# Optimization experiments

Measured on AMD Instinct MI355X. Metric: run time of the kernel, lower is better.

Reference implementation:

```python
import jax, jax.numpy as jnp
import numpy as np

B, H, KLEN, D = 32, 8, 8192, 64  # batch, heads, kv_len, head_dim


def setup_inputs() -> dict:
    key = jax.random.key(0)
    k1, k2, k3, k4 = jax.random.split(key, 4)
    std = 1.0 / D ** 0.5
    Q = jax.random.normal(k1, (B, H, 1, D), dtype=jnp.float32)
    K = jax.random.normal(k2, (B, H, KLEN, D), dtype=jnp.float32)
    W_c = jax.random.normal(k3, (H, 2 * D, D), dtype=jnp.float32) * std
    W_o = jax.random.normal(k4, (H, D, 1), dtype=jnp.float32) * std
    bias = jnp.zeros((H, 1, D), dtype=jnp.float32)
    return {"Q": Q, "K": K, "W_c": W_c, "W_o": W_o, "bias": bias}


def reference(Q, K, W_c, W_o, bias):
    # concat score (NAIS, He et al. 2018)
    Qe = jnp.broadcast_to(Q, K.shape)                       # [b,h,k,d]
    QK_cat = jnp.concatenate([Qe, K], axis=-1)              # [b,h,k,2d]
    hidden = jax.nn.relu(
        jnp.einsum('bhke,hed->bhkd', QK_cat, W_c) + bias    # bias [h,1,d] broadcasts
    )                                                        # [b,h,k,d]
    scores = jnp.einsum('bhkd,hde->bhk', hidden, W_o)       # sums over d and e(=1)
    return scores
```

## Files before the change

kernel.cpp:

```cpp
#include <hip/hip_runtime.h>
#include <stdint.h>

#define B_    32
#define H_    8
#define KLEN_ 8192
#define D_    64
#define SPLIT 8
#define ROWS_PER_BLOCK (KLEN_ / SPLIT)
#define WAVES 4
#define ITERS (ROWS_PER_BLOCK / (WAVES * 16))

typedef __attribute__((ext_vector_type(8))) short short8;
typedef __attribute__((ext_vector_type(4))) float float4v;

static __device__ inline unsigned short f2bf(float f) {
    uint32_t u = __builtin_bit_cast(uint32_t, f);
    u += 0x7fffu + ((u >> 16) & 1u);
    return (unsigned short)(u >> 16);
}

__global__ __launch_bounds__(256) void nais_score_kernel(
    const float* __restrict__ Q,
    const float* __restrict__ K,
    const float* __restrict__ Wc,
    const float* __restrict__ Wo,
    const float* __restrict__ bias,
    float* __restrict__ out)
{
    const int blk   = blockIdx.x;
    const int bh    = blk / SPLIT;
    const int split = blk % SPLIT;
    const int h     = bh % H_;
    const int tid   = threadIdx.x;
    const int lane  = tid & 63;
    const int wave  = tid >> 6;
    const int c     = lane & 15;
    const int q     = lane >> 4;

    __shared__ float s_qb[D_];
    __shared__ float s_wo[D_];

    if (tid < D_) {
        const float* qv = Q + (size_t)bh * D_;
        const float* wq = Wc + (size_t)h * (2 * D_ * D_);
        float acc = bias[h * D_ + tid];
        #pragma unroll 8
        for (int e = 0; e < D_; ++e)
            acc += qv[e] * wq[e * D_ + tid];
        s_qb[tid] = acc;
        s_wo[tid] = Wo[h * D_ + tid];
    }
    __syncthreads();

    const float* wk = Wc + (size_t)h * (2 * D_ * D_) + D_ * D_;
    short8 bfrag[4][2];
    #pragma unroll
    for (int t = 0; t < 4; ++t) {
        const int d = t * 16 + c;
        #pragma unroll
        for (int half = 0; half < 2; ++half) {
            short8 f;
            #pragma unroll
            for (int j = 0; j < 8; ++j) {
                const int e = half * 32 + q * 8 + j;
                f[j] = (short)f2bf(wk[e * D_ + d]);
            }
            bfrag[t][half] = f;
        }
    }

    float qbl[4], wol[4];
    #pragma unroll
    for (int t = 0; t < 4; ++t) {
        qbl[t] = s_qb[t * 16 + c];
        wol[t] = s_wo[t * 16 + c];
    }

    const float* Kb = K + (size_t)bh * KLEN_ * D_ + (size_t)split * ROWS_PER_BLOCK * D_;
    float*       ob = out + (size_t)bh * KLEN_ + (size_t)split * ROWS_PER_BLOCK;

    for (int it = 0; it < ITERS; ++it) {
        const int krow = (it * WAVES + wave) * 16;
        const float* arow = Kb + (size_t)(krow + c) * D_ + q * 8;
        float4v a0lo = *(const float4v*)(arow);
        float4v a0hi = *(const float4v*)(arow + 4);
        float4v a1lo = *(const float4v*)(arow + 32);
        float4v a1hi = *(const float4v*)(arow + 36);
        short8 af0, af1;
        #pragma unroll
        for (int j = 0; j < 4; ++j) {
            af0[j]     = (short)f2bf(a0lo[j]);
            af0[j + 4] = (short)f2bf(a0hi[j]);
            af1[j]     = (short)f2bf(a1lo[j]);
            af1[j + 4] = (short)f2bf(a1hi[j]);
        }

        float4v pr = {0.f, 0.f, 0.f, 0.f};
        #pragma unroll
        for (int t = 0; t < 4; ++t) {
            float4v acc = {0.f, 0.f, 0.f, 0.f};
            acc = __builtin_amdgcn_mfma_f32_16x16x32_bf16(af0, bfrag[t][0], acc, 0, 0, 0);
            acc = __builtin_amdgcn_mfma_f32_16x16x32_bf16(af1, bfrag[t][1], acc, 0, 0, 0);
            #pragma unroll
            for (int r = 0; r < 4; ++r) {
                float hv = acc[r] + qbl[t];
                hv = fmaxf(hv, 0.f);
                pr[r] += hv * wol[t];
            }
        }

        #pragma unroll
        for (int r = 0; r < 4; ++r) {
            float v = pr[r];
            v += __shfl_xor(v, 1);
            v += __shfl_xor(v, 2);
            v += __shfl_xor(v, 4);
            v += __shfl_xor(v, 8);
            if (c == r) ob[krow + q * 4 + r] = v;
        }
    }
}

extern "C" void kernel_launch(void* const* d_in, const int* in_sizes, int n_in,
                              void* d_out, int out_size, void* d_ws, size_t ws_size,
                              hipStream_t stream) {
    const float* Q    = (const float*)d_in[0];
    const float* K    = (const float*)d_in[1];
    const float* Wc   = (const float*)d_in[2];
    const float* Wo   = (const float*)d_in[3];
    const float* bias = (const float*)d_in[4];
    float* out = (float*)d_out;

    dim3 grid(B_ * H_ * SPLIT);
    dim3 block(256);
    nais_score_kernel<<<grid, block, 0, stream>>>(Q, K, Wc, Wo, bias, out);
}
```

Measured before the change: 694.8 us.

## Coalesce K loads via LDS transpose, prefetch next tile, double split count

Each wave now reads its 16-row K tile with fully coalesced contiguous float4 loads, converts to bf16 with a cheaper round-half-up pack via v_perm, and writes the tile into a padded per-wave LDS buffer. It then reads MFMA A-fragments back from LDS. The next tile is register-prefetched while the current one is processed, and SPLIT doubles to launch more blocks. This targets memory latency and uncoalesced global access in a bandwidth-bound kernel, at the cost of LDS traffic. The bf16 rounding changes slightly from round-to-nearest-even to round-half-up.

```diff
diff --git a/kernel.cpp b/kernel.cpp
--- a/kernel.cpp
+++ b/kernel.cpp
@@ -5,18 +5,22 @@
 #define H_    8
 #define KLEN_ 8192
 #define D_    64
-#define SPLIT 8
+#define SPLIT 16
 #define ROWS_PER_BLOCK (KLEN_ / SPLIT)
 #define WAVES 4
-#define ITERS (ROWS_PER_BLOCK / (WAVES * 16))
+#define TILES (ROWS_PER_BLOCK / (WAVES * 16))
+
+#define LDS_ROW 144
 
 typedef __attribute__((ext_vector_type(8))) short short8;
 typedef __attribute__((ext_vector_type(4))) float float4v;
+typedef __attribute__((ext_vector_type(4))) unsigned int uint4v;
+typedef __attribute__((ext_vector_type(2))) unsigned int uint2v;
 
-static __device__ inline unsigned short f2bf(float f) {
-    uint32_t u = __builtin_bit_cast(uint32_t, f);
-    u += 0x7fffu + ((u >> 16) & 1u);
-    return (unsigned short)(u >> 16);
+static __device__ inline unsigned int pack_bf16(float x0, float x1) {
+    unsigned int a = __builtin_bit_cast(unsigned int, x0) + 0x8000u;
+    unsigned int b = __builtin_bit_cast(unsigned int, x1) + 0x8000u;
+    return __builtin_amdgcn_perm(b, a, 0x07060302u);
 }
 
 __global__ __launch_bounds__(256) void nais_score_kernel(
@@ -39,6 +43,7 @@
 
     __shared__ float s_qb[D_];
     __shared__ float s_wo[D_];
+    __shared__ unsigned char s_tile[WAVES][16 * LDS_ROW] __attribute__((aligned(16)));
 
     if (tid < D_) {
         const float* qv = Q + (size_t)bh * D_;
@@ -59,13 +64,13 @@
         const int d = t * 16 + c;
         #pragma unroll
         for (int half = 0; half < 2; ++half) {
-            short8 f;
+            uint4v f;
             #pragma unroll
-            for (int j = 0; j < 8; ++j) {
-                const int e = half * 32 + q * 8 + j;
-                f[j] = (short)f2bf(wk[e * D_ + d]);
+            for (int j2 = 0; j2 < 4; ++j2) {
+                const int e = half * 32 + q * 8 + 2 * j2;
+                f[j2] = pack_bf16(wk[(size_t)e * D_ + d], wk[(size_t)(e + 1) * D_ + d]);
             }
-            bfrag[t][half] = f;
+            bfrag[t][half] = __builtin_bit_cast(short8, f);
         }
     }
 
@@ -78,37 +83,49 @@
 
     const float* Kb = K + (size_t)bh * KLEN_ * D_ + (size_t)split * ROWS_PER_BLOCK * D_;
     float*       ob = out + (size_t)bh * KLEN_ + (size_t)split * ROWS_PER_BLOCK;
+    unsigned char* myTile = s_tile[wave];
 
-    for (int it = 0; it < ITERS; ++it) {
-        const int krow = (it * WAVES + wave) * 16;
-        const float* arow = Kb + (size_t)(krow + c) * D_ + q * 8;
-        float4v a0lo = *(const float4v*)(arow);
-        float4v a0hi = *(const float4v*)(arow + 4);
-        float4v a1lo = *(const float4v*)(arow + 32);
-        float4v a1hi = *(const float4v*)(arow + 36);
-        short8 af0, af1;
+    #define TILE_PTR(t) (Kb + (size_t)(((t) * WAVES + wave) * 16) * D_)
+
+    float4v st[2][4];
+    #pragma unroll
+    for (int j = 0; j < 4; ++j)
+        st[0][j] = *(const float4v*)(TILE_PTR(0) + j * 256 + lane * 4);
+
+    for (int t = 0; t < TILES; ++t) {
+        const int cb = t & 1, nb = cb ^ 1;
+        if (t + 1 < TILES) {
+            #pragma unroll
+            for (int j = 0; j < 4; ++j)
+                st[nb][j] = *(const float4v*)(TILE_PTR(t + 1) + j * 256 + lane * 4);
+        }
+
         #pragma unroll
         for (int j = 0; j < 4; ++j) {
-            af0[j]     = (short)f2bf(a0lo[j]);
-            af0[j + 4] = (short)f2bf(a0hi[j]);
-            af1[j]     = (short)f2bf(a1lo[j]);
-            af1[j + 4] = (short)f2bf(a1hi[j]);
+            const int r = j * 4 + q;
+            uint2v w;
+            w[0] = pack_bf16(st[cb][j][0], st[cb][j][1]);
+            w[1] = pack_bf16(st[cb][j][2], st[cb][j][3]);
+            *(uint2v*)(myTile + r * LDS_ROW + c * 8) = w;
         }
+
+        short8 af0 = *(const short8*)(myTile + c * LDS_ROW + q * 16);
+        short8 af1 = *(const short8*)(myTile + c * LDS_ROW + 64 + q * 16);
 
         float4v pr = {0.f, 0.f, 0.f, 0.f};
         #pragma unroll
-        for (int t = 0; t < 4; ++t) {
+        for (int tt = 0; tt < 4; ++tt) {
             float4v acc = {0.f, 0.f, 0.f, 0.f};
-            acc = __builtin_amdgcn_mfma_f32_16x16x32_bf16(af0, bfrag[t][0], acc, 0, 0, 0);
-            acc = __builtin_amdgcn_mfma_f32_16x16x32_bf16(af1, bfrag[t][1], acc, 0, 0, 0);
+            acc = __builtin_amdgcn_mfma_f32_16x16x32_bf16(af0, bfrag[tt][0], acc, 0, 0, 0);
+            acc = __builtin_amdgcn_mfma_f32_16x16x32_bf16(af1, bfrag[tt][1], acc, 0, 0, 0);
             #pragma unroll
             for (int r = 0; r < 4; ++r) {
-                float hv = acc[r] + qbl[t];
-                hv = fmaxf(hv, 0.f);
-                pr[r] += hv * wol[t];
+                float hv = fmaxf(acc[r] + qbl[tt], 0.f);
+                pr[r] += hv * wol[tt];
             }
         }
 
+        const int krow = (t * WAVES + wave) * 16;
         #pragma unroll
         for (int r = 0; r < 4; ++r) {
             float v = pr[r];
@@ -119,6 +136,7 @@
             if (c == r) ob[krow + q * 4 + r] = v;
         }
     }
+    #undef TILE_PTR
 }
 
 extern "C" void kernel_launch(void* const* d_in, const int* in_sizes, int n_in,
```

After: 692.7 us. Within noise of the previous version (-0.3%).
